# Performance work log

Measured on AMD Instinct MI355X. Metric: run time of the kernel, lower is better.

## Reference

```python
import jax, jax.numpy as jnp
import numpy as np

WDIM = 16
NBATCH = 1024
N = 4096
DF = 2 * WDIM  # Wishart degrees of freedom


def setup_inputs() -> dict:
    key = jax.random.key(0)
    k1, k2, k3 = jax.random.split(key, 3)
    # strict-lower-triangular noise for the Bartlett factor
    A_noise = jax.random.normal(k1, (NBATCH, WDIM, WDIM), dtype=jnp.float32)
    # Chi2(df - i) draws for the diagonal: chi2(k) = 2 * Gamma(k/2)
    a = (DF - jnp.arange(WDIM, dtype=jnp.float32)) / 2.0  # [wdim]
    chisq = (2.0 * jax.random.gamma(k2, a, (NBATCH, WDIM))).astype(jnp.float32)
    # final standard-normal draw applied to the normalized inverse factor
    z = jax.random.normal(k3, (NBATCH, N, WDIM), dtype=jnp.float32)
    return {"A_noise": A_noise, "chisq": chisq, "z": z}


def reference(A_noise, chisq, z):
    # Bartlett cholesky factor of Wishart(I, 2*wdim): lower-tri with sqrt(chi2) diag.
    # (V = I so L = chol(V) = I and the original L @ A is a no-op.)
    eye = jnp.eye(WDIM, dtype=A_noise.dtype)
    A = jnp.tril(A_noise, -1) + jnp.sqrt(chisq)[:, :, None] * eye  # [b, p, p]
    # A = inverse(sample).transpose(-2, -1)
    At = jnp.swapaxes(jnp.linalg.inv(A), -1, -2)  # [b, p, p]
    # diag(At @ At^T)^(-1/2) = rsqrt of row norms squared
    scale = jax.lax.rsqrt(jnp.sum(At * At, axis=-1))  # [b, p]
    M = scale[:, :, None] * At  # diag_embed(scale) @ At, [b, p, p]
    # w = (M broadcast over n) @ z[..., None], squeezed -> [b, n, p]
    w = jnp.einsum('bij,bnj->bni', M, z)
    return w
```

## Files before the change

kernel.cpp:

```cpp
#include <hip/hip_runtime.h>

#define NB 1024
#define NN 4096
#define P  16

__global__ __launch_bounds__(256) void build_M(const float* __restrict__ A_noise,
                                               const float* __restrict__ chisq,
                                               float* __restrict__ M) {
  __shared__ float As[16][P][17];
  __shared__ float colS[256][17];

  const int tid = threadIdx.x;
  const int lb  = tid >> 4;
  const int j   = tid & 15;
  const int b   = blockIdx.x * 16 + lb;

  {
    const float* src = A_noise + (size_t)blockIdx.x * 16 * P * P + (size_t)tid * P;
    for (int v = 0; v < P; ++v) As[tid >> 4][tid & 15][v] = src[v];
  }
  __syncthreads();

  const float* cs = chisq + (size_t)b * P;
  float* col = colS[tid];

  const float cj = rsqrtf(cs[j]);
  col[j] = cj;
  float n2 = cj * cj;
  for (int i = j + 1; i < P; ++i) {
    float s = 0.f;
    for (int k = j; k < i; ++k) s += As[lb][i][k] * col[k];
    const float ci = -s * rsqrtf(cs[i]);
    col[i] = ci;
    n2 += ci * ci;
  }
  const float sc = rsqrtf(n2);

  float* Mb = M + (size_t)b * P * P + (size_t)j * P;
  for (int i = 0; i < j; ++i) Mb[i] = 0.f;
  for (int i = j; i < P; ++i) Mb[i] = sc * col[i];
}

#define TPB 256
#define RPT 8
#define SEGB (NN * 4)
#define BPB  (SEGB / (TPB * RPT))

__global__ __launch_bounds__(TPB) void apply_M(const float* __restrict__ M,
                                               const float* __restrict__ z,
                                               float* __restrict__ w) {
  const int b     = blockIdx.x >> 3;
  const int chunk = blockIdx.x & 7;
  const int tid   = threadIdx.x;
  const int q     = tid & 3;
  const int quad0 = tid & ~3;

  const float4* Mf4 = (const float4*)(M + (size_t)b * P * P);
  float4 Mr[4][4];
#pragma unroll
  for (int c = 0; c < 4; ++c)
#pragma unroll
    for (int s = 0; s < 4; ++s) Mr[c][s] = Mf4[(4 * q + c) * 4 + s];

  const size_t segbase = (size_t)b * SEGB + (size_t)chunk * (TPB * RPT) + tid;
  const float4* zf4 = (const float4*)z;
  float4* wf4 = (float4*)w;

  float4 zv[RPT];
#pragma unroll
  for (int k = 0; k < RPT; ++k) zv[k] = zf4[segbase + (size_t)k * TPB];

#pragma unroll
  for (int k = 0; k < RPT; ++k) {
    float4 row[4];
#pragma unroll
    for (int d = 0; d < 4; ++d) {
      row[d].x = __shfl(zv[k].x, quad0 + d, 64);
      row[d].y = __shfl(zv[k].y, quad0 + d, 64);
      row[d].z = __shfl(zv[k].z, quad0 + d, 64);
      row[d].w = __shfl(zv[k].w, quad0 + d, 64);
    }
    float out[4];
#pragma unroll
    for (int c = 0; c < 4; ++c) {
      float acc = 0.f;
#pragma unroll
      for (int s = 0; s < 4; ++s) {
        acc = fmaf(Mr[c][s].x, row[s].x, acc);
        acc = fmaf(Mr[c][s].y, row[s].y, acc);
        acc = fmaf(Mr[c][s].z, row[s].z, acc);
        acc = fmaf(Mr[c][s].w, row[s].w, acc);
      }
      out[c] = acc;
    }
    wf4[segbase + (size_t)k * TPB] = make_float4(out[0], out[1], out[2], out[3]);
  }
}

extern "C" void kernel_launch(void* const* d_in, const int* in_sizes, int n_in,
                              void* d_out, int out_size, void* d_ws, size_t ws_size,
                              hipStream_t stream) {
  const float* A_noise = (const float*)d_in[0];
  const float* chisq   = (const float*)d_in[1];
  const float* z       = (const float*)d_in[2];
  float* wv = (float*)d_out;
  float* Mw = (float*)d_ws;

  build_M<<<NB / 16, 256, 0, stream>>>(A_noise, chisq, Mw);
  apply_M<<<NB * BPB, TPB, 0, stream>>>(Mw, z, wv);
}
```

Baseline: 442.7 us.

## Fuse M construction into apply kernel with nontemporal z loads and w stores

Merges the two kernels into one: every block recomputes its batch's 16x16 normalized inverse factor in shared memory (16 threads do the triangular solve) and then applies it to its z chunk. The z loads are issued before the solve so the memory latency overlaps the serial solve. Loads and stores now use nontemporal builtins. This removes a kernel launch and the workspace round-trip for M, at the cost of recomputing M 8 times per batch and two block barriers.

```diff
diff --git a/kernel.cpp b/kernel.cpp
--- a/kernel.cpp
+++ b/kernel.cpp
@@ -3,76 +3,67 @@
 #define NB 1024
 #define NN 4096
 #define P  16
-
-__global__ __launch_bounds__(256) void build_M(const float* __restrict__ A_noise,
-                                               const float* __restrict__ chisq,
-                                               float* __restrict__ M) {
-  __shared__ float As[16][P][17];
-  __shared__ float colS[256][17];
-
-  const int tid = threadIdx.x;
-  const int lb  = tid >> 4;
-  const int j   = tid & 15;
-  const int b   = blockIdx.x * 16 + lb;
-
-  {
-    const float* src = A_noise + (size_t)blockIdx.x * 16 * P * P + (size_t)tid * P;
-    for (int v = 0; v < P; ++v) As[tid >> 4][tid & 15][v] = src[v];
-  }
-  __syncthreads();
-
-  const float* cs = chisq + (size_t)b * P;
-  float* col = colS[tid];
-
-  const float cj = rsqrtf(cs[j]);
-  col[j] = cj;
-  float n2 = cj * cj;
-  for (int i = j + 1; i < P; ++i) {
-    float s = 0.f;
-    for (int k = j; k < i; ++k) s += As[lb][i][k] * col[k];
-    const float ci = -s * rsqrtf(cs[i]);
-    col[i] = ci;
-    n2 += ci * ci;
-  }
-  const float sc = rsqrtf(n2);
-
-  float* Mb = M + (size_t)b * P * P + (size_t)j * P;
-  for (int i = 0; i < j; ++i) Mb[i] = 0.f;
-  for (int i = j; i < P; ++i) Mb[i] = sc * col[i];
-}
-
 #define TPB 256
 #define RPT 8
 #define SEGB (NN * 4)
 #define BPB  (SEGB / (TPB * RPT))
 
-__global__ __launch_bounds__(TPB) void apply_M(const float* __restrict__ M,
-                                               const float* __restrict__ z,
-                                               float* __restrict__ w) {
+typedef float f4 __attribute__((ext_vector_type(4)));
+
+__global__ __launch_bounds__(TPB) void prior_w_fused(
+    const float* __restrict__ A_noise, const float* __restrict__ chisq,
+    const float* __restrict__ z, float* __restrict__ w) {
+  __shared__ __align__(16) float Msh[P][P];
+  __shared__ float As[P][P + 1];
+  __shared__ float colS[P][P + 1];
+  __shared__ float dS[P];
+
+  const int tid   = threadIdx.x;
   const int b     = blockIdx.x >> 3;
   const int chunk = blockIdx.x & 7;
-  const int tid   = threadIdx.x;
   const int q     = tid & 3;
   const int quad0 = tid & ~3;
 
-  const float4* Mf4 = (const float4*)(M + (size_t)b * P * P);
-  float4 Mr[4][4];
+  const size_t segbase = (size_t)b * SEGB + (size_t)chunk * (TPB * RPT) + tid;
+  const f4* zf4 = (const f4*)z;
+  f4 zv[RPT];
+#pragma unroll
+  for (int k = 0; k < RPT; ++k)
+    zv[k] = __builtin_nontemporal_load(zf4 + segbase + (size_t)k * TPB);
+
+  As[tid >> 4][tid & 15] = A_noise[(size_t)b * (P * P) + tid];
+  if (tid < P) dS[tid] = rsqrtf(chisq[(size_t)b * P + tid]);
+  __syncthreads();
+
+  if (tid < P) {
+    const int j = tid;
+    const float cj = dS[j];
+    colS[j][j] = cj;
+    float n2 = cj * cj;
+    for (int i = j + 1; i < P; ++i) {
+      float s = 0.f;
+      for (int k = j; k < i; ++k) s += As[i][k] * colS[j][k];
+      const float ci = -s * dS[i];
+      colS[j][i] = ci;
+      n2 += ci * ci;
+    }
+    const float sc = rsqrtf(n2);
+    for (int i = 0; i < j; ++i) Msh[j][i] = 0.f;
+    for (int i = j; i < P; ++i) Msh[j][i] = sc * colS[j][i];
+  }
+  __syncthreads();
+
+  f4 Mr[4][4];
 #pragma unroll
   for (int c = 0; c < 4; ++c)
 #pragma unroll
-    for (int s = 0; s < 4; ++s) Mr[c][s] = Mf4[(4 * q + c) * 4 + s];
+    for (int s = 0; s < 4; ++s)
+      Mr[c][s] = *(const f4*)&Msh[4 * q + c][4 * s];
 
-  const size_t segbase = (size_t)b * SEGB + (size_t)chunk * (TPB * RPT) + tid;
-  const float4* zf4 = (const float4*)z;
-  float4* wf4 = (float4*)w;
-
-  float4 zv[RPT];
-#pragma unroll
-  for (int k = 0; k < RPT; ++k) zv[k] = zf4[segbase + (size_t)k * TPB];
-
+  f4* wf4 = (f4*)w;
 #pragma unroll
   for (int k = 0; k < RPT; ++k) {
-    float4 row[4];
+    f4 row[4];
 #pragma unroll
     for (int d = 0; d < 4; ++d) {
       row[d].x = __shfl(zv[k].x, quad0 + d, 64);
@@ -80,7 +71,7 @@
       row[d].z = __shfl(zv[k].z, quad0 + d, 64);
       row[d].w = __shfl(zv[k].w, quad0 + d, 64);
     }
-    float out[4];
+    f4 o;
 #pragma unroll
     for (int c = 0; c < 4; ++c) {
       float acc = 0.f;
@@ -91,9 +82,10 @@
         acc = fmaf(Mr[c][s].z, row[s].z, acc);
         acc = fmaf(Mr[c][s].w, row[s].w, acc);
       }
-      out[c] = acc;
+      if (c == 0) o.x = acc; else if (c == 1) o.y = acc;
+      else if (c == 2) o.z = acc; else o.w = acc;
     }
-    wf4[segbase + (size_t)k * TPB] = make_float4(out[0], out[1], out[2], out[3]);
+    __builtin_nontemporal_store(o, wf4 + segbase + (size_t)k * TPB);
   }
 }
 
@@ -103,9 +95,5 @@
   const float* A_noise = (const float*)d_in[0];
   const float* chisq   = (const float*)d_in[1];
   const float* z       = (const float*)d_in[2];
-  float* wv = (float*)d_out;
-  float* Mw = (float*)d_ws;
-
-  build_M<<<NB / 16, 256, 0, stream>>>(A_noise, chisq, Mw);
-  apply_M<<<NB * BPB, TPB, 0, stream>>>(Mw, z, wv);
+  prior_w_fused<<<NB * BPB, TPB, 0, stream>>>(A_noise, chisq, z, (float*)d_out);
 }
```

New measurement: 441.9 us. No clear change (-0.2%).
